# Performance work log

Hardware: AMD Instinct MI355X
Metric: run time of the kernel (lower is better)

## Reference

```python
import jax, jax.numpy as jnp
import numpy as np

N0, N1, N2 = 120000, 24000, 6000  # nodes per sampled layer
H1, C1 = 8, 64   # layer1: heads, nhid (concat -> 512)
H2, C2 = 8, 256  # layer2: out heads, code_embed_dim (mean over heads)
D = 256
NEG_SLOPE = 0.2


def gat_conv(x_src, x_dst, src, dst, W, att_src, att_dst, bias, n_tgt, concat):
    H, C = att_src.shape
    h_src = (x_src @ W).reshape(-1, H, C)   # [N_src, H, C]
    h_dst = (x_dst @ W).reshape(-1, H, C)   # [N_tgt, H, C]
    a_src = jnp.einsum('nhc,hc->nh', h_src, att_src)  # [N_src, H]
    a_dst = jnp.einsum('nhc,hc->nh', h_dst, att_dst)  # [N_tgt, H]
    e = a_src[src] + a_dst[dst]                       # [E, H]
    e = jnp.where(e > 0, e, NEG_SLOPE * e)            # LeakyReLU
    # segment softmax over edges grouped by target node
    m = jax.ops.segment_max(e, dst, num_segments=n_tgt)  # [N_tgt, H]
    ex = jnp.exp(e - m[dst])
    denom = jax.ops.segment_sum(ex, dst, num_segments=n_tgt)
    alpha = ex / denom[dst]                           # [E, H]
    msg = alpha[:, :, None] * h_src[src]              # [E, H, C]
    out = jax.ops.segment_sum(msg, dst, num_segments=n_tgt)  # [N_tgt, H, C]
    if concat:
        return out.reshape(n_tgt, H * C) + bias
    return out.mean(axis=1) + bias


def setup_inputs() -> dict:
    key = jax.random.key(0)
    ks = jax.random.split(key, 12)
    E1, E2 = 384000, 96000
    g1 = 1.0 / np.sqrt(D)
    g2 = 1.0 / np.sqrt(H1 * C1)
    return {
        'x': jax.random.normal(ks[0], (N0, D), jnp.float32),
        'src1': jax.random.randint(ks[1], (E1,), 0, N0),
        'dst1': jax.random.randint(ks[2], (E1,), 0, N1),
        'src2': jax.random.randint(ks[3], (E2,), 0, N1),
        'dst2': jax.random.randint(ks[4], (E2,), 0, N2),
        'W1': jax.random.normal(ks[5], (D, H1 * C1), jnp.float32) * g1,
        'att_src1': jax.random.normal(ks[6], (H1, C1), jnp.float32) * 0.1,
        'att_dst1': jax.random.normal(ks[7], (H1, C1), jnp.float32) * 0.1,
        'b1': jnp.zeros((H1 * C1,), jnp.float32),
        'W2': jax.random.normal(ks[8], (H1 * C1, H2 * C2), jnp.float32) * g2,
        'att_src2': jax.random.normal(ks[9], (H2, C2), jnp.float32) * 0.1,
        'att_dst2': jax.random.normal(ks[10], (H2, C2), jnp.float32) * 0.1,
        'b2': jnp.zeros((C2,), jnp.float32),
    }


def reference(x, src1, dst1, src2, dst2, W1, att_src1, att_dst1, b1,
              W2, att_src2, att_dst2, b2):
    # layer 1: bipartite conv (x, x[:N1]), concat heads, then ELU
    x1 = gat_conv(x, x[:N1], src1, dst1, W1, att_src1, att_dst1, b1, N1, True)
    x1 = jax.nn.elu(x1)
    # layer 2: (x1, x1[:N2]), mean over heads
    x2 = gat_conv(x1, x1[:N2], src2, dst2, W2, att_src2, att_dst2, b2, N2, False)
    return x2
```

## Files before the change

### kernel.cpp

```cpp
#include <hip/hip_runtime.h>
#include <hip/hip_bf16.h>
#include <cstdint>

typedef __attribute__((ext_vector_type(8))) short short8;
typedef __attribute__((ext_vector_type(4))) float floatx4;
typedef __hip_bfloat16 bf16;
typedef unsigned short u16;

static constexpr int cN0 = 120000, cN1 = 24000, cN2 = 6000;
static constexpr int cD = 256, cHC1 = 512;
static constexpr int CH1 = 4800;

__device__ __forceinline__ float dot4(float4 a, float4 b) {
  return a.x * b.x + a.y * b.y + a.z * b.z + a.w * b.w;
}

__global__ __launch_bounds__(256)
void gat_w1t(const float* __restrict__ W1, u16* __restrict__ dst) {
  int t = blockIdx.x * 256 + threadIdx.x;
  if (t >= 512 * 256) return;
  int n = t >> 8, k = t & 255;
  bf16 v = bf16(W1[(size_t)k * 512 + n]);
  dst[t] = *(u16*)&v;
}

__global__ __launch_bounds__(256)
void gat_make_w2te(const float* __restrict__ W2, u16* __restrict__ out) {
  __shared__ u16 tile[32][33];
  int kt = blockIdx.x * 32, ct = blockIdx.y * 32, h = blockIdx.z;
  int tx = threadIdx.x & 31, ty4 = (threadIdx.x >> 5) * 4;
#pragma unroll
  for (int i = 0; i < 4; i++) {
    int k = kt + ty4 + i, c = ct + tx;
    bf16 v = bf16(W2[(size_t)k * 2048 + h * 256 + c]);
    tile[ty4 + i][tx] = *(u16*)&v;
  }
  __syncthreads();
#pragma unroll
  for (int i = 0; i < 4; i++) {
    int c = ct + ty4 + i, k = kt + tx;
    out[(size_t)c * 4096 + h * 512 + k] = tile[tx][ty4 + i];
  }
}

__global__ __launch_bounds__(256)
void gat_make_watt(const float* __restrict__ W, const float* __restrict__ atts,
                   const float* __restrict__ attd, float* __restrict__ ws,
                   float* __restrict__ wd, int K, int Ch, int ldw) {
  int lane = threadIdx.x & 63;
  int task = blockIdx.x * 4 + (threadIdx.x >> 6);
  if (task >= 8 * K) return;
  int h = task / K, k = task - h * K;
  const float* Wr = W + (size_t)k * ldw + h * Ch;
  const float* as = atts + h * Ch;
  const float* ad = attd + h * Ch;
  float ss = 0.f, dd = 0.f;
  for (int c = lane; c < Ch; c += 64) {
    float wv = Wr[c];
    ss += wv * as[c];
    dd += wv * ad[c];
  }
#pragma unroll
  for (int o = 32; o; o >>= 1) { ss += __shfl_down(ss, o); dd += __shfl_down(dd, o); }
  if (lane == 0) { ws[task] = ss; wd[task] = dd; }
}

#define RSTAGE(HALF, MASK)                                              \
  {                                                                     \
    _Pragma("unroll") for (int j = 0; j < HALF; j++) {                  \
      float send = (lane & MASK) ? v[j] : v[j + HALF];                  \
      float rcv = __shfl_xor(send, MASK);                               \
      v[j] = ((lane & MASK) ? v[j + HALF] : v[j]) + rcv;                \
    }                                                                   \
  }

__global__ __launch_bounds__(256)
void gat_scores_reg(const float* __restrict__ x, const float* __restrict__ wsrc,
                    const float* __restrict__ wdst, float* __restrict__ a_s,
                    float* __restrict__ a_d, int M, int MD) {
  int lane = threadIdx.x & 63;
  int wv = (blockIdx.x * 256 + threadIdx.x) >> 6;
  int nw = (gridDim.x * 256) >> 6;
  float4 w[16];
#pragma unroll
  for (int j = 0; j < 8; j++) {
    w[j]     = *(const float4*)&wsrc[j * 256 + lane * 4];
    w[j + 8] = *(const float4*)&wdst[j * 256 + lane * 4];
  }
  for (int row = wv; row < M; row += nw) {
    float4 xv = *(const float4*)&x[(size_t)row * 256 + lane * 4];
    float v[16];
#pragma unroll
    for (int j = 0; j < 16; j++) v[j] = dot4(xv, w[j]);
    RSTAGE(8, 1) RSTAGE(4, 2) RSTAGE(2, 4) RSTAGE(1, 8)
    v[0] += __shfl_xor(v[0], 16);
    v[0] += __shfl_xor(v[0], 32);
    if (lane < 16) {
      int o = ((lane & 1) << 3) | ((lane & 2) << 1) | ((lane & 4) >> 1) | ((lane & 8) >> 3);
      if (o < 8) a_s[row * 8 + o] = v[0];
      else if (row < MD) a_d[row * 8 + (o - 8)] = v[0];
    }
  }
}

__global__ __launch_bounds__(256)
void gat_scores_w512(const float* __restrict__ x, const float* __restrict__ wsrc,
                     const float* __restrict__ wdst, float* __restrict__ a_s,
                     float* __restrict__ a_d, int M, int MD) {
  __shared__ float wl[16 * 512];
  int tid = threadIdx.x;
#pragma unroll
  for (int base = 0; base < 8192; base += 1024) {
    int idx = base + tid * 4;
    int j = idx >> 9, c = idx & 511;
    *(float4*)&wl[idx] = (j < 8) ? *(const float4*)&wsrc[j * 512 + c]
                                 : *(const float4*)&wdst[(j - 8) * 512 + c];
  }
  __syncthreads();
  int lane = tid & 63;
  int wv = (blockIdx.x * 256 + tid) >> 6;
  int nw = (gridDim.x * 256) >> 6;
  for (int row = wv; row < M; row += nw) {
    float4 xa = *(const float4*)&x[(size_t)row * 512 + lane * 4];
    float4 xb = *(const float4*)&x[(size_t)row * 512 + 256 + lane * 4];
    float v[16];
#pragma unroll
    for (int j = 0; j < 16; j++) {
      float4 wa = *(const float4*)&wl[j * 512 + lane * 4];
      float4 wb = *(const float4*)&wl[j * 512 + 256 + lane * 4];
      v[j] = dot4(xa, wa) + dot4(xb, wb);
    }
    RSTAGE(8, 1) RSTAGE(4, 2) RSTAGE(2, 4) RSTAGE(1, 8)
    v[0] += __shfl_xor(v[0], 16);
    v[0] += __shfl_xor(v[0], 32);
    if (lane < 16) {
      int o = ((lane & 1) << 3) | ((lane & 2) << 1) | ((lane & 4) >> 1) | ((lane & 8) >> 3);
      if (o < 8) a_s[row * 8 + o] = v[0];
      else if (row < MD) a_d[row * 8 + (o - 8)] = v[0];
    }
  }
}

__global__ __launch_bounds__(256)
void gat_hist(const int* __restrict__ dstv, int* __restrict__ cnt, int E) {
  int t = blockIdx.x * 256 + threadIdx.x;
  if (t < E) atomicAdd(&cnt[dstv[t]], 1);
}

__global__ __launch_bounds__(1024)
void gat_scan1(const int* __restrict__ cnt, int* __restrict__ off,
               int* __restrict__ bsum, int n) {
  __shared__ int wsum[16];
  int t = threadIdx.x, lane = t & 63, wid = t >> 6;
  int idx = blockIdx.x * 1024 + t;
  int v = (idx < n) ? cnt[idx] : 0;
  int x = v;
#pragma unroll
  for (int d = 1; d < 64; d <<= 1) { int y = __shfl_up(x, d); if (lane >= d) x += y; }
  if (lane == 63) wsum[wid] = x;
  __syncthreads();
  if (t < 16) {
    int s = wsum[t];
#pragma unroll
    for (int d = 1; d < 16; d <<= 1) { int y = __shfl_up(s, d); if (t >= d) s += y; }
    wsum[t] = s;
  }
  __syncthreads();
  int excl = (wid ? wsum[wid - 1] : 0) + x - v;
  if (idx < n) off[idx] = excl;
  if (t == 1023) bsum[blockIdx.x] = wsum[15];
}

__global__ __launch_bounds__(64)
void gat_scan2(int* __restrict__ bsum, int nb, int* __restrict__ off, int n) {
  int t = threadIdx.x;
  int v = (t < nb) ? bsum[t] : 0;
  int x = v;
#pragma unroll
  for (int d = 1; d < 64; d <<= 1) { int y = __shfl_up(x, d); if (t >= d) x += y; }
  if (t < nb) bsum[t] = x - v;
  if (t == 63) off[n] = x;
}

__global__ __launch_bounds__(256)
void gat_scan3(int* __restrict__ off, const int* __restrict__ bsum, int n) {
  int i = blockIdx.x * 256 + threadIdx.x;
  if (i < n) off[i] += bsum[i >> 10];
}

__global__ __launch_bounds__(256)
void gat_scatter_edge(const int* __restrict__ src, const int* __restrict__ dstv,
                      const float* __restrict__ a_s, const float* __restrict__ a_d,
                      const int* __restrict__ off, int* __restrict__ cur,
                      int* __restrict__ srcs, float* __restrict__ exs, int E) {
  int t = blockIdx.x * 256 + threadIdx.x;
  if (t >= E) return;
  int s = src[t], d = dstv[t];
  int slot = off[d] + atomicAdd(&cur[d], 1);
  srcs[slot] = s;
  const float* as = a_s + (size_t)s * 8;
  const float* ad = a_d + (size_t)d * 8;
  float4 s0 = *(const float4*)as, s1 = *(const float4*)(as + 4);
  float4 d0 = *(const float4*)ad, d1 = *(const float4*)(ad + 4);
  float ev[8] = { s0.x + d0.x, s0.y + d0.y, s0.z + d0.z, s0.w + d0.w,
                  s1.x + d1.x, s1.y + d1.y, s1.z + d1.z, s1.w + d1.w };
  float exv[8];
#pragma unroll
  for (int h = 0; h < 8; h++) {
    float e = ev[h];
    e = e > 0.f ? e : 0.2f * e;
    exv[h] = expf(e);
  }
  float4* op = (float4*)(exs + (size_t)slot * 8);
  op[0] = make_float4(exv[0], exv[1], exv[2], exv[3]);
  op[1] = make_float4(exv[4], exv[5], exv[6], exv[7]);
}

__global__ __launch_bounds__(256)
void gat_gather_in1(const float* __restrict__ x, const float* __restrict__ exs,
                    const int* __restrict__ off, const int* __restrict__ srcs,
                    u16* __restrict__ agg, int d0) {
  int d = d0 + blockIdx.x, t = threadIdx.x;
  int beg = off[d], end = off[d + 1];
  float acc[8] = {}, den[8] = {};
  int i = beg;
  if ((end - beg) & 1) {
    int s = srcs[i];
    float ea[8];
    *(float4*)&ea[0] = *(const float4*)&exs[(size_t)i * 8];
    *(float4*)&ea[4] = *(const float4*)&exs[(size_t)i * 8 + 4];
    float xv = x[(size_t)s * cD + t];
#pragma unroll
    for (int j = 0; j < 8; j++) { acc[j] += ea[j] * xv; den[j] += ea[j]; }
    i++;
  }
  for (; i < end; i += 2) {
    int s0 = srcs[i], s1 = srcs[i + 1];
    float ea[8], eb[8];
    *(float4*)&ea[0] = *(const float4*)&exs[(size_t)i * 8];
    *(float4*)&ea[4] = *(const float4*)&exs[(size_t)i * 8 + 4];
    *(float4*)&eb[0] = *(const float4*)&exs[(size_t)(i + 1) * 8];
    *(float4*)&eb[4] = *(const float4*)&exs[(size_t)(i + 1) * 8 + 4];
    float xv0 = x[(size_t)s0 * cD + t];
    float xv1 = x[(size_t)s1 * cD + t];
#pragma unroll
    for (int j = 0; j < 8; j++) {
      acc[j] += ea[j] * xv0 + eb[j] * xv1;
      den[j] += ea[j] + eb[j];
    }
  }
  u16* ap = agg + (size_t)blockIdx.x * 2048 + t;
#pragma unroll
  for (int j = 0; j < 8; j++) {
    float inv = den[j] > 0.f ? 1.f / den[j] : 0.f;
    bf16 v = bf16(acc[j] * inv);
    ap[(size_t)j * 256] = *(u16*)&v;
  }
}

__global__ __launch_bounds__(256)
void gat_gather_in2(const float* __restrict__ x1, const float* __restrict__ exs,
                    const int* __restrict__ off, const int* __restrict__ srcs,
                    u16* __restrict__ agg, int d0) {
  int d = d0 + blockIdx.x, t = threadIdx.x;
  int beg = off[d], end = off[d + 1];
  float acc0[8] = {}, acc1[8] = {}, den[8] = {};
  int i = beg;
  if ((end - beg) & 1) {
    int s = srcs[i];
    float ea[8];
    *(float4*)&ea[0] = *(const float4*)&exs[(size_t)i * 8];
    *(float4*)&ea[4] = *(const float4*)&exs[(size_t)i * 8 + 4];
    float xa = x1[(size_t)s * cHC1 + t];
    float xb = x1[(size_t)s * cHC1 + t + 256];
#pragma unroll
    for (int j = 0; j < 8; j++) { acc0[j] += ea[j] * xa; acc1[j] += ea[j] * xb; den[j] += ea[j]; }
    i++;
  }
  for (; i < end; i += 2) {
    int s0 = srcs[i], s1 = srcs[i + 1];
    float ea[8], eb[8];
    *(float4*)&ea[0] = *(const float4*)&exs[(size_t)i * 8];
    *(float4*)&ea[4] = *(const float4*)&exs[(size_t)i * 8 + 4];
    *(float4*)&eb[0] = *(const float4*)&exs[(size_t)(i + 1) * 8];
    *(float4*)&eb[4] = *(const float4*)&exs[(size_t)(i + 1) * 8 + 4];
    float xa0 = x1[(size_t)s0 * cHC1 + t];
    float xb0 = x1[(size_t)s0 * cHC1 + t + 256];
    float xa1 = x1[(size_t)s1 * cHC1 + t];
    float xb1 = x1[(size_t)s1 * cHC1 + t + 256];
#pragma unroll
    for (int j = 0; j < 8; j++) {
      acc0[j] += ea[j] * xa0 + eb[j] * xa1;
      acc1[j] += ea[j] * xb0 + eb[j] * xb1;
      den[j] += ea[j] + eb[j];
    }
  }
  u16* ap = agg + (size_t)blockIdx.x * 4096;
#pragma unroll
  for (int j = 0; j < 8; j++) {
    float inv = den[j] > 0.f ? 1.f / den[j] : 0.f;
    bf16 v0 = bf16(acc0[j] * inv), v1 = bf16(acc1[j] * inv);
    ap[(size_t)j * 512 + t]       = *(u16*)&v0;
    ap[(size_t)j * 512 + t + 256] = *(u16*)&v1;
  }
}

template<int BN, int EPI>
__global__ __launch_bounds__(256)
void gat_gemm(const u16* __restrict__ A, long lda, const u16* __restrict__ Bt, long ldb,
              float* __restrict__ C, long ldc, int M, int K,
              const float* __restrict__ bias, int zA, int zB, long zC, int zBias) {
  __shared__ __align__(16) u16 Al[64 * 64];
  __shared__ __align__(16) u16 Bl[BN * 64];
  const int tid = threadIdx.x;
  const int bm = blockIdx.x << 6;
  const int n0 = blockIdx.y * BN;
  const int z = blockIdx.z;
  const u16* Ab = A + (size_t)z * zA;
  const u16* Bb = Bt + (size_t)z * zB + (size_t)n0 * ldb;
  const int wid = tid >> 6, lane = tid & 63;
  const int wm = (wid & 1) << 5, wn = (wid >> 1) * (BN / 2);
  const int q = lane >> 4, r = lane & 15;
  constexpr int NJ = BN / 32;
  floatx4 acc[2][NJ] = {};
  const int arow = tid >> 3;
  const int chunk = tid & 7;
  const int acol = chunk << 3;
  for (int k0 = 0; k0 < K; k0 += 64) {
    __syncthreads();
#pragma unroll
    for (int rr = 0; rr < 2; rr++) {
      int row = arow + rr * 32;
      int gr = bm + row; if (gr >= M) gr = M - 1;
      *(uint4*)&Al[row * 64 + ((chunk ^ (row & 7)) << 3)] =
          *(const uint4*)&Ab[(size_t)gr * lda + k0 + acol];
    }
#pragma unroll
    for (int rr = 0; rr < BN / 32; rr++) {
      int row = arow + rr * 32;
      *(uint4*)&Bl[row * 64 + ((chunk ^ (row & 7)) << 3)] =
          *(const uint4*)&Bb[(size_t)row * ldb + k0 + acol];
    }
    __syncthreads();
#pragma unroll
    for (int kk = 0; kk < 64; kk += 32) {
      const int cs = (((kk >> 3) + q) ^ (r & 7)) << 3;
      short8 af[2], bfr[NJ];
#pragma unroll
      for (int i = 0; i < 2; i++)  af[i]  = *(const short8*)&Al[(wm + i * 16 + r) * 64 + cs];
#pragma unroll
      for (int j = 0; j < NJ; j++) bfr[j] = *(const short8*)&Bl[(wn + j * 16 + r) * 64 + cs];
#pragma unroll
      for (int i = 0; i < 2; i++)
#pragma unroll
        for (int j = 0; j < NJ; j++)
          acc[i][j] = __builtin_amdgcn_mfma_f32_16x16x32_bf16(af[i], bfr[j], acc[i][j], 0, 0, 0);
    }
  }
#pragma unroll
  for (int i = 0; i < 2; i++)
#pragma unroll
    for (int j = 0; j < NJ; j++) {
      int gn = n0 + wn + j * 16 + r;
      float bv = (EPI == 1) ? bias[zBias * z + gn] : 0.f;
#pragma unroll
      for (int t2 = 0; t2 < 4; t2++) {
        int gm = bm + wm + i * 16 + q * 4 + t2;
        if (gm < M) {
          float v = acc[i][j][t2];
          if (EPI == 1) { v += bv; v = v > 0.f ? v : expm1f(v); }
          C[(size_t)z * zC + (size_t)gm * ldc + gn] = v;
        }
      }
    }
}

__global__ __launch_bounds__(256)
void gat_reduce4(const float* __restrict__ p, const float* __restrict__ bias,
                 float* __restrict__ out, int MN) {
  int t = blockIdx.x * 256 + threadIdx.x;
  if (t >= MN) return;
  size_t mn = (size_t)MN;
  float v = p[t] + p[t + mn] + p[t + 2 * mn] + p[t + 3 * mn];
  out[t] = v * 0.125f + bias[t & 255];
}

extern "C" void kernel_launch(void* const* d_in, const int* in_sizes, int n_in,
                              void* d_out, int out_size, void* d_ws, size_t ws_size,
                              hipStream_t stream) {
  const float* x    = (const float*)d_in[0];
  const int* src1   = (const int*)d_in[1];
  const int* dst1   = (const int*)d_in[2];
  const int* src2   = (const int*)d_in[3];
  const int* dst2   = (const int*)d_in[4];
  const float* W1   = (const float*)d_in[5];
  const float* atts1 = (const float*)d_in[6];
  const float* attd1 = (const float*)d_in[7];
  const float* b1   = (const float*)d_in[8];
  const float* W2   = (const float*)d_in[9];
  const float* atts2 = (const float*)d_in[10];
  const float* attd2 = (const float*)d_in[11];
  const float* b2   = (const float*)d_in[12];
  const int E1 = in_sizes[1], E2 = in_sizes[3];

  uint8_t* p = (uint8_t*)d_ws;
  auto alloc = [&](size_t b) { uint8_t* r = p; p += (b + 255) & ~(size_t)255; return r; };
  auto al = [](size_t b) { return (b + 255) & ~(size_t)255; };
  float* x1   = (float*)alloc((size_t)cN1 * cHC1 * 4);
  u16*   W1t  = (u16*)alloc((size_t)512 * 256 * 2);
  u16*   W2te = (u16*)alloc((size_t)256 * 4096 * 2);
  float* wts1 = (float*)alloc(8 * 256 * 4);
  float* wtd1 = (float*)alloc(8 * 256 * 4);
  float* wts2 = (float*)alloc(8 * 512 * 4);
  float* wtd2 = (float*)alloc(8 * 512 * 4);
  uint8_t* scratch = p;
  size_t usedPersist = (size_t)(scratch - (uint8_t*)d_ws);

  auto phaseA = [&](size_t m1) {
    return al(m1 * 2048 * 2) + al((size_t)cN0 * 32) + al((size_t)cN1 * 32) +
           al((size_t)E1 * 32) + al((size_t)E1 * 4) + al((size_t)(cN1 + 1) * 4) +
           al(256) + 2 * al((size_t)cN1 * 4);
  };
  int M1 = (usedPersist + phaseA(cN1) <= ws_size) ? cN1 : CH1;
  int nch1 = cN1 / M1;
  u16*   aggA  = (u16*)alloc((size_t)M1 * 2048 * 2);
  float* a_s1  = (float*)alloc((size_t)cN0 * 32);
  float* a_d1  = (float*)alloc((size_t)cN1 * 32);
  float* exs1  = (float*)alloc((size_t)E1 * 32);
  int*   srcs1 = (int*)alloc((size_t)E1 * 4);
  int*   off1  = (int*)alloc((size_t)(cN1 + 1) * 4);
  int*   bsum1 = (int*)alloc(256);
  uint8_t* zA = p;
  int*   cnt1 = (int*)alloc((size_t)cN1 * 4);
  int*   cur1 = (int*)alloc((size_t)cN1 * 4);
  size_t zAbytes = (size_t)(p - zA);

  auto phaseB = [&](size_t m2) {
    return al(m2 * 4096 * 2) + al(4ull * m2 * 256 * 4) + al((size_t)cN1 * 32) +
           al((size_t)cN2 * 32) + al((size_t)E2 * 32) + al((size_t)E2 * 4) +
           al((size_t)(cN2 + 1) * 4) + al(256) + 2 * al((size_t)cN2 * 4);
  };
  int M2 = (usedPersist + phaseB(6000) <= ws_size) ? 6000 : 3000;
  int nch2 = 6000 / M2;
  p = scratch;
  u16*   aggB  = (u16*)alloc((size_t)M2 * 4096 * 2);
  float* pbuf  = (float*)alloc(4ull * M2 * 256 * 4);
  float* a_s2  = (float*)alloc((size_t)cN1 * 32);
  float* a_d2  = (float*)alloc((size_t)cN2 * 32);
  float* exs2  = (float*)alloc((size_t)E2 * 32);
  int*   srcs2 = (int*)alloc((size_t)E2 * 4);
  int*   off2  = (int*)alloc((size_t)(cN2 + 1) * 4);
  int*   bsum2 = (int*)alloc(256);
  uint8_t* zB = p;
  int*   cnt2 = (int*)alloc((size_t)cN2 * 4);
  int*   cur2 = (int*)alloc((size_t)cN2 * 4);
  size_t zBbytes = (size_t)(p - zB);

  gat_w1t<<<(512 * 256 + 255) / 256, 256, 0, stream>>>(W1, W1t);
  gat_make_w2te<<<dim3(16, 8, 8), 256, 0, stream>>>(W2, W2te);
  gat_make_watt<<<2 * 256, 256, 0, stream>>>(W1, atts1, attd1, wts1, wtd1, 256, 64, 512);
  gat_make_watt<<<2 * 512, 256, 0, stream>>>(W2, atts2, attd2, wts2, wtd2, 512, 256, 2048);

  hipMemsetAsync(zA, 0, zAbytes, stream);
  gat_scores_reg<<<1024, 256, 0, stream>>>(x, wts1, wtd1, a_s1, a_d1, cN0, cN1);
  gat_hist<<<(E1 + 255) / 256, 256, 0, stream>>>(dst1, cnt1, E1);
  {
    int nb = (cN1 + 1023) / 1024;
    gat_scan1<<<nb, 1024, 0, stream>>>(cnt1, off1, bsum1, cN1);
    gat_scan2<<<1, 64, 0, stream>>>(bsum1, nb, off1, cN1);
    gat_scan3<<<(cN1 + 255) / 256, 256, 0, stream>>>(off1, bsum1, cN1);
  }
  gat_scatter_edge<<<(E1 + 255) / 256, 256, 0, stream>>>(src1, dst1, a_s1, a_d1, off1, cur1, srcs1, exs1, E1);
  for (int c = 0; c < nch1; c++) {
    int d0 = c * M1;
    gat_gather_in1<<<M1, 256, 0, stream>>>(x, exs1, off1, srcs1, aggA, d0);
    gat_gemm<64, 1><<<dim3(M1 / 64, 1, 8), 256, 0, stream>>>(
        aggA, 2048, W1t, 256, x1 + (size_t)d0 * cHC1, cHC1,
        M1, 256, b1, 256, 64 * 256, 64, 64);
  }

  hipMemsetAsync(zB, 0, zBbytes, stream);
  gat_scores_w512<<<512, 256, 0, stream>>>(x1, wts2, wtd2, a_s2, a_d2, cN1, cN2);
  gat_hist<<<(E2 + 255) / 256, 256, 0, stream>>>(dst2, cnt2, E2);
  {
    int nb = (cN2 + 1023) / 1024;
    gat_scan1<<<nb, 1024, 0, stream>>>(cnt2, off2, bsum2, cN2);
    gat_scan2<<<1, 64, 0, stream>>>(bsum2, nb, off2, cN2);
    gat_scan3<<<(cN2 + 255) / 256, 256, 0, stream>>>(off2, bsum2, cN2);
  }
  gat_scatter_edge<<<(E2 + 255) / 256, 256, 0, stream>>>(src2, dst2, a_s2, a_d2, off2, cur2, srcs2, exs2, E2);
  for (int c = 0; c < nch2; c++) {
    int d0 = c * M2;
    gat_gather_in2<<<M2, 256, 0, stream>>>(x1, exs2, off2, srcs2, aggB, d0);
    gat_gemm<128, 0><<<dim3((M2 + 63) / 64, 2, 4), 256, 0, stream>>>(
        aggB, 4096, W2te, 4096, pbuf, 256,
        M2, 1024, nullptr, 1024, 1024, (long)M2 * 256, 0);
    gat_reduce4<<<(M2 * 256 + 255) / 256, 256, 0, stream>>>(
        pbuf, b2, (float*)d_out + (size_t)d0 * 256, M2 * 256);
  }
}
```

Measured before the change: 495.4 us.

## Merge prep kernels, fold scan stages, split softmax denominator from gather

Combines the four weight-preparation kernels into one launch and merges the second and third scan stages so each block sums the per-block partials itself. It also moves the softmax denominator into a separate per-node kernel and rewrites the gather as one templated kernel that unrolls four edges per iteration. Layer 2 now uses 512 threads per node instead of two columns per thread. The intent is to cut launch count and raise memory-level parallelism in the gathers, at the cost of an extra denominator pass and extra den buffers.

Measured after the change: 483.9 us. 2.3% less time.

```diff
diff --git a/kernel.cpp b/kernel.cpp
--- a/kernel.cpp
+++ b/kernel.cpp
@@ -16,49 +16,63 @@
 }
 
 __global__ __launch_bounds__(256)
-void gat_w1t(const float* __restrict__ W1, u16* __restrict__ dst) {
-  int t = blockIdx.x * 256 + threadIdx.x;
-  if (t >= 512 * 256) return;
-  int n = t >> 8, k = t & 255;
-  bf16 v = bf16(W1[(size_t)k * 512 + n]);
-  dst[t] = *(u16*)&v;
-}
-
-__global__ __launch_bounds__(256)
-void gat_make_w2te(const float* __restrict__ W2, u16* __restrict__ out) {
+void gat_prep(const float* __restrict__ W1, const float* __restrict__ W2,
+              const float* __restrict__ as1, const float* __restrict__ ad1,
+              const float* __restrict__ as2, const float* __restrict__ ad2,
+              u16* __restrict__ W1t, u16* __restrict__ W2te,
+              float* __restrict__ wts1, float* __restrict__ wtd1,
+              float* __restrict__ wts2, float* __restrict__ wtd2) {
   __shared__ u16 tile[32][33];
-  int kt = blockIdx.x * 32, ct = blockIdx.y * 32, h = blockIdx.z;
-  int tx = threadIdx.x & 31, ty4 = (threadIdx.x >> 5) * 4;
-#pragma unroll
-  for (int i = 0; i < 4; i++) {
-    int k = kt + ty4 + i, c = ct + tx;
-    bf16 v = bf16(W2[(size_t)k * 2048 + h * 256 + c]);
-    tile[ty4 + i][tx] = *(u16*)&v;
-  }
-  __syncthreads();
-#pragma unroll
-  for (int i = 0; i < 4; i++) {
-    int c = ct + ty4 + i, k = kt + tx;
-    out[(size_t)c * 4096 + h * 512 + k] = tile[tx][ty4 + i];
-  }
-}
-
-__global__ __launch_bounds__(256)
-void gat_make_watt(const float* __restrict__ W, const float* __restrict__ atts,
-                   const float* __restrict__ attd, float* __restrict__ ws,
-                   float* __restrict__ wd, int K, int Ch, int ldw) {
+  int b = (int)blockIdx.x;
+  if (b < 512) {
+    int t = b * 256 + threadIdx.x;
+    int n = t >> 8, k = t & 255;
+    bf16 v = bf16(W1[(size_t)k * 512 + n]);
+    W1t[t] = *(u16*)&v;
+    return;
+  }
+  b -= 512;
+  if (b < 1024) {
+    int bx = b & 15, by = (b >> 4) & 7, h = b >> 7;
+    int kt = bx * 32, ct = by * 32;
+    int tx = threadIdx.x & 31, ty4 = (threadIdx.x >> 5) * 4;
+#pragma unroll
+    for (int i = 0; i < 4; i++) {
+      int k = kt + ty4 + i, c = ct + tx;
+      bf16 v = bf16(W2[(size_t)k * 2048 + h * 256 + c]);
+      tile[ty4 + i][tx] = *(u16*)&v;
+    }
+    __syncthreads();
+#pragma unroll
+    for (int i = 0; i < 4; i++) {
+      int c = ct + ty4 + i, k = kt + tx;
+      W2te[(size_t)c * 4096 + h * 512 + k] = tile[tx][ty4 + i];
+    }
+    return;
+  }
+  b -= 1024;
   int lane = threadIdx.x & 63;
-  int task = blockIdx.x * 4 + (threadIdx.x >> 6);
+  int K, Ch, ldw, task;
+  const float *W, *as, *ad;
+  float *ws, *wd;
+  if (b < 512) {
+    K = 256; Ch = 64; ldw = 512; W = W1; as = as1; ad = ad1; ws = wts1; wd = wtd1;
+    task = b * 4 + (threadIdx.x >> 6);
+  } else {
+    b -= 512;
+    K = 512; Ch = 256; ldw = 2048; W = W2; as = as2; ad = ad2; ws = wts2; wd = wtd2;
+    task = b * 4 + (threadIdx.x >> 6);
+  }
   if (task >= 8 * K) return;
   int h = task / K, k = task - h * K;
   const float* Wr = W + (size_t)k * ldw + h * Ch;
-  const float* as = atts + h * Ch;
-  const float* ad = attd + h * Ch;
+  const float* asp = as + h * Ch;
+  const float* adp = ad + h * Ch;
   float ss = 0.f, dd = 0.f;
   for (int c = lane; c < Ch; c += 64) {
     float wv = Wr[c];
-    ss += wv * as[c];
-    dd += wv * ad[c];
+    ss += wv * asp[c];
+    dd += wv * adp[c];
   }
 #pragma unroll
   for (int o = 32; o; o >>= 1) { ss += __shfl_down(ss, o); dd += __shfl_down(dd, o); }
@@ -171,21 +185,18 @@
   if (t == 1023) bsum[blockIdx.x] = wsum[15];
 }
 
-__global__ __launch_bounds__(64)
-void gat_scan2(int* __restrict__ bsum, int nb, int* __restrict__ off, int n) {
-  int t = threadIdx.x;
-  int v = (t < nb) ? bsum[t] : 0;
-  int x = v;
-#pragma unroll
-  for (int d = 1; d < 64; d <<= 1) { int y = __shfl_up(x, d); if (t >= d) x += y; }
-  if (t < nb) bsum[t] = x - v;
-  if (t == 63) off[n] = x;
-}
-
-__global__ __launch_bounds__(256)
-void gat_scan3(int* __restrict__ off, const int* __restrict__ bsum, int n) {
+__global__ __launch_bounds__(256)
+void gat_scan3(int* __restrict__ off, const int* __restrict__ bsum, int n, int nb) {
   int i = blockIdx.x * 256 + threadIdx.x;
-  if (i < n) off[i] += bsum[i >> 10];
+  int blk = (blockIdx.x * 256) >> 10;
+  int add = 0;
+  for (int b = 0; b < blk; b++) add += bsum[b];
+  if (i < n) off[i] += add;
+  if (i == 0) {
+    int tot = 0;
+    for (int b = 0; b < nb; b++) tot += bsum[b];
+    off[n] = tot;
+  }
 }
 
 __global__ __launch_bounds__(256)
@@ -217,91 +228,72 @@
 }
 
 __global__ __launch_bounds__(256)
-void gat_gather_in1(const float* __restrict__ x, const float* __restrict__ exs,
-                    const int* __restrict__ off, const int* __restrict__ srcs,
-                    u16* __restrict__ agg, int d0) {
+void gat_denom(const float* __restrict__ exs, const int* __restrict__ off,
+               float* __restrict__ den, int N) {
+  int lane = threadIdx.x & 63;
+  int d = blockIdx.x * 4 + (threadIdx.x >> 6);
+  if (d >= N) return;
+  int beg = off[d], end = off[d + 1];
+  float s = 0.f;
+  for (size_t idx = (size_t)beg * 8 + lane; idx < (size_t)end * 8; idx += 64)
+    s += exs[idx];
+#pragma unroll
+  for (int o = 32; o >= 8; o >>= 1) s += __shfl_down(s, o);
+  if (lane < 8) den[(size_t)d * 8 + lane] = s;
+}
+
+template<int CDIM>
+__global__ __launch_bounds__(CDIM)
+void gat_gather(const float* __restrict__ x, const float* __restrict__ exs,
+                const float* __restrict__ den, const int* __restrict__ off,
+                const int* __restrict__ srcs, u16* __restrict__ agg, int d0) {
   int d = d0 + blockIdx.x, t = threadIdx.x;
   int beg = off[d], end = off[d + 1];
-  float acc[8] = {}, den[8] = {};
+  float inv[8];
+#pragma unroll
+  for (int j = 0; j < 8; j++) {
+    float dv = den[(size_t)d * 8 + j];
+    inv[j] = dv > 0.f ? 1.f / dv : 0.f;
+  }
+  float acc[8] = {};
+  const float* xb = x + t;
   int i = beg;
-  if ((end - beg) & 1) {
+  for (; i + 4 <= end; i += 4) {
+    int s0 = srcs[i], s1 = srcs[i + 1], s2 = srcs[i + 2], s3 = srcs[i + 3];
+    float xv0 = xb[(size_t)s0 * CDIM];
+    float xv1 = xb[(size_t)s1 * CDIM];
+    float xv2 = xb[(size_t)s2 * CDIM];
+    float xv3 = xb[(size_t)s3 * CDIM];
+    float4 e0a = *(const float4*)&exs[(size_t)i * 8];
+    float4 e0b = *(const float4*)&exs[(size_t)i * 8 + 4];
+    float4 e1a = *(const float4*)&exs[(size_t)(i + 1) * 8];
+    float4 e1b = *(const float4*)&exs[(size_t)(i + 1) * 8 + 4];
+    float4 e2a = *(const float4*)&exs[(size_t)(i + 2) * 8];
+    float4 e2b = *(const float4*)&exs[(size_t)(i + 2) * 8 + 4];
+    float4 e3a = *(const float4*)&exs[(size_t)(i + 3) * 8];
+    float4 e3b = *(const float4*)&exs[(size_t)(i + 3) * 8 + 4];
+    acc[0] += e0a.x * xv0 + e1a.x * xv1 + e2a.x * xv2 + e3a.x * xv3;
+    acc[1] += e0a.y * xv0 + e1a.y * xv1 + e2a.y * xv2 + e3a.y * xv3;
+    acc[2] += e0a.z * xv0 + e1a.z * xv1 + e2a.z * xv2 + e3a.z * xv3;
+    acc[3] += e0a.w * xv0 + e1a.w * xv1 + e2a.w * xv2 + e3a.w * xv3;
+    acc[4] += e0b.x * xv0 + e1b.x * xv1 + e2b.x * xv2 + e3b.x * xv3;
+    acc[5] += e0b.y * xv0 + e1b.y * xv1 + e2b.y * xv2 + e3b.y * xv3;
+    acc[6] += e0b.z * xv0 + e1b.z * xv1 + e2b.z * xv2 + e3b.z * xv3;
+    acc[7] += e0b.w * xv0 + e1b.w * xv1 + e2b.w * xv2 + e3b.w * xv3;
+  }
+  for (; i < end; i++) {
     int s = srcs[i];
-    float ea[8];
-    *(float4*)&ea[0] = *(const float4*)&exs[(size_t)i * 8];
-    *(float4*)&ea[4] = *(const float4*)&exs[(size_t)i * 8 + 4];
-    float xv = x[(size_t)s * cD + t];
-#pragma unroll
-    for (int j = 0; j < 8; j++) { acc[j] += ea[j] * xv; den[j] += ea[j]; }
-    i++;
-  }
-  for (; i < end; i += 2) {
-    int s0 = srcs[i], s1 = srcs[i + 1];
-    float ea[8], eb[8];
-    *(float4*)&ea[0] = *(const float4*)&exs[(size_t)i * 8];
-    *(float4*)&ea[4] = *(const float4*)&exs[(size_t)i * 8 + 4];
-    *(float4*)&eb[0] = *(const float4*)&exs[(size_t)(i + 1) * 8];
-    *(float4*)&eb[4] = *(const float4*)&exs[(size_t)(i + 1) * 8 + 4];
-    float xv0 = x[(size_t)s0 * cD + t];
-    float xv1 = x[(size_t)s1 * cD + t];
-#pragma unroll
-    for (int j = 0; j < 8; j++) {
-      acc[j] += ea[j] * xv0 + eb[j] * xv1;
-      den[j] += ea[j] + eb[j];
-    }
-  }
-  u16* ap = agg + (size_t)blockIdx.x * 2048 + t;
+    float xv = xb[(size_t)s * CDIM];
+    float4 ea = *(const float4*)&exs[(size_t)i * 8];
+    float4 eb = *(const float4*)&exs[(size_t)i * 8 + 4];
+    acc[0] += ea.x * xv; acc[1] += ea.y * xv; acc[2] += ea.z * xv; acc[3] += ea.w * xv;
+    acc[4] += eb.x * xv; acc[5] += eb.y * xv; acc[6] += eb.z * xv; acc[7] += eb.w * xv;
+  }
+  u16* ap = agg + (size_t)blockIdx.x * (8 * CDIM) + t;
 #pragma unroll
   for (int j = 0; j < 8; j++) {
-    float inv = den[j] > 0.f ? 1.f / den[j] : 0.f;
-    bf16 v = bf16(acc[j] * inv);
-    ap[(size_t)j * 256] = *(u16*)&v;
-  }
-}
-
-__global__ __launch_bounds__(256)
-void gat_gather_in2(const float* __restrict__ x1, const float* __restrict__ exs,
-                    const int* __restrict__ off, const int* __restrict__ srcs,
-                    u16* __restrict__ agg, int d0) {
-  int d = d0 + blockIdx.x, t = threadIdx.x;
-  int beg = off[d], end = off[d + 1];
-  float acc0[8] = {}, acc1[8] = {}, den[8] = {};
-  int i = beg;
-  if ((end - beg) & 1) {
-    int s = srcs[i];
-    float ea[8];
-    *(float4*)&ea[0] = *(const float4*)&exs[(size_t)i * 8];
-    *(float4*)&ea[4] = *(const float4*)&exs[(size_t)i * 8 + 4];
-    float xa = x1[(size_t)s * cHC1 + t];
-    float xb = x1[(size_t)s * cHC1 + t + 256];
-#pragma unroll
-    for (int j = 0; j < 8; j++) { acc0[j] += ea[j] * xa; acc1[j] += ea[j] * xb; den[j] += ea[j]; }
-    i++;
-  }
-  for (; i < end; i += 2) {
-    int s0 = srcs[i], s1 = srcs[i + 1];
-    float ea[8], eb[8];
-    *(float4*)&ea[0] = *(const float4*)&exs[(size_t)i * 8];
-    *(float4*)&ea[4] = *(const float4*)&exs[(size_t)i * 8 + 4];
-    *(float4*)&eb[0] = *(const float4*)&exs[(size_t)(i + 1) * 8];
-    *(float4*)&eb[4] = *(const float4*)&exs[(size_t)(i + 1) * 8 + 4];
-    float xa0 = x1[(size_t)s0 * cHC1 + t];
-    float xb0 = x1[(size_t)s0 * cHC1 + t + 256];
-    float xa1 = x1[(size_t)s1 * cHC1 + t];
-    float xb1 = x1[(size_t)s1 * cHC1 + t + 256];
-#pragma unroll
-    for (int j = 0; j < 8; j++) {
-      acc0[j] += ea[j] * xa0 + eb[j] * xa1;
-      acc1[j] += ea[j] * xb0 + eb[j] * xb1;
-      den[j] += ea[j] + eb[j];
-    }
-  }
-  u16* ap = agg + (size_t)blockIdx.x * 4096;
-#pragma unroll
-  for (int j = 0; j < 8; j++) {
-    float inv = den[j] > 0.f ? 1.f / den[j] : 0.f;
-    bf16 v0 = bf16(acc0[j] * inv), v1 = bf16(acc1[j] * inv);
-    ap[(size_t)j * 512 + t]       = *(u16*)&v0;
-    ap[(size_t)j * 512 + t + 256] = *(u16*)&v1;
+    bf16 v = bf16(acc[j] * inv[j]);
+    ap[(size_t)j * CDIM] = *(u16*)&v;
   }
 }
 
@@ -419,7 +411,7 @@
   auto phaseA = [&](size_t m1) {
     return al(m1 * 2048 * 2) + al((size_t)cN0 * 32) + al((size_t)cN1 * 32) +
            al((size_t)E1 * 32) + al((size_t)E1 * 4) + al((size_t)(cN1 + 1) * 4) +
-           al(256) + 2 * al((size_t)cN1 * 4);
+           al(256) + al((size_t)cN1 * 32) + 2 * al((size_t)cN1 * 4);
   };
   int M1 = (usedPersist + phaseA(cN1) <= ws_size) ? cN1 : CH1;
   int nch1 = cN1 / M1;
@@ -430,6 +422,7 @@
   int*   srcs1 = (int*)alloc((size_t)E1 * 4);
   int*   off1  = (int*)alloc((size_t)(cN1 + 1) * 4);
   int*   bsum1 = (int*)alloc(256);
+  float* den1  = (float*)alloc((size_t)cN1 * 32);
   uint8_t* zA = p;
   int*   cnt1 = (int*)alloc((size_t)cN1 * 4);
   int*   cur1 = (int*)alloc((size_t)cN1 * 4);
@@ -438,7 +431,8 @@
   auto phaseB = [&](size_t m2) {
     return al(m2 * 4096 * 2) + al(4ull * m2 * 256 * 4) + al((size_t)cN1 * 32) +
            al((size_t)cN2 * 32) + al((size_t)E2 * 32) + al((size_t)E2 * 4) +
-           al((size_t)(cN2 + 1) * 4) + al(256) + 2 * al((size_t)cN2 * 4);
+           al((size_t)(cN2 + 1) * 4) + al(256) + al((size_t)cN2 * 32) +
+           2 * al((size_t)cN2 * 4);
   };
   int M2 = (usedPersist + phaseB(6000) <= ws_size) ? 6000 : 3000;
   int nch2 = 6000 / M2;
@@ -451,15 +445,14 @@
   int*   srcs2 = (int*)alloc((size_t)E2 * 4);
   int*   off2  = (int*)alloc((size_t)(cN2 + 1) * 4);
   int*   bsum2 = (int*)alloc(256);
+  float* den2  = (float*)alloc((size_t)cN2 * 32);
   uint8_t* zB = p;
   int*   cnt2 = (int*)alloc((size_t)cN2 * 4);
   int*   cur2 = (int*)alloc((size_t)cN2 * 4);
   size_t zBbytes = (size_t)(p - zB);
 
-  gat_w1t<<<(512 * 256 + 255) / 256, 256, 0, stream>>>(W1, W1t);
-  gat_make_w2te<<<dim3(16, 8, 8), 256, 0, stream>>>(W2, W2te);
-  gat_make_watt<<<2 * 256, 256, 0, stream>>>(W1, atts1, attd1, wts1, wtd1, 256, 64, 512);
-  gat_make_watt<<<2 * 512, 256, 0, stream>>>(W2, atts2, attd2, wts2, wtd2, 512, 256, 2048);
+  gat_prep<<<3072, 256, 0, stream>>>(W1, W2, atts1, attd1, atts2, attd2,
+                                     W1t, W2te, wts1, wtd1, wts2, wtd2);
 
   hipMemsetAsync(zA, 0, zAbytes, stream);
   gat_scores_reg<<<1024, 256, 0, stream>>>(x, wts1, wtd1, a_s1, a_d1, cN0, cN1);
@@ -467,13 +460,13 @@
   {
     int nb = (cN1 + 1023) / 1024;
     gat_scan1<<<nb, 1024, 0, stream>>>(cnt1, off1, bsum1, cN1);
-    gat_scan2<<<1, 64, 0, stream>>>(bsum1, nb, off1, cN1);
-    gat_scan3<<<(cN1 + 255) / 256, 256, 0, stream>>>(off1, bsum1, cN1);
+    gat_scan3<<<(cN1 + 255) / 256, 256, 0, stream>>>(off1, bsum1, cN1, nb);
   }
   gat_scatter_edge<<<(E1 + 255) / 256, 256, 0, stream>>>(src1, dst1, a_s1, a_d1, off1, cur1, srcs1, exs1, E1);
+  gat_denom<<<(cN1 + 3) / 4, 256, 0, stream>>>(exs1, off1, den1, cN1);
   for (int c = 0; c < nch1; c++) {
     int d0 = c * M1;
-    gat_gather_in1<<<M1, 256, 0, stream>>>(x, exs1, off1, srcs1, aggA, d0);
+    gat_gather<256><<<M1, 256, 0, stream>>>(x, exs1, den1, off1, srcs1, aggA, d0);
     gat_gemm<64, 1><<<dim3(M1 / 64, 1, 8), 256, 0, stream>>>(
         aggA, 2048, W1t, 256, x1 + (size_t)d0 * cHC1, cHC1,
         M1, 256, b1, 256, 64 * 256, 64, 64);
@@ -485,13 +478,13 @@
   {
     int nb = (cN2 + 1023) / 1024;
     gat_scan1<<<nb, 1024, 0, stream>>>(cnt2, off2, bsum2, cN2);
-    gat_scan2<<<1, 64, 0, stream>>>(bsum2, nb, off2, cN2);
-    gat_scan3<<<(cN2 + 255) / 256, 256, 0, stream>>>(off2, bsum2, cN2);
+    gat_scan3<<<(cN2 + 255) / 256, 256, 0, stream>>>(off2, bsum2, cN2, nb);
   }
   gat_scatter_edge<<<(E2 + 255) / 256, 256, 0, stream>>>(src2, dst2, a_s2, a_d2, off2, cur2, srcs2, exs2, E2);
+  gat_denom<<<(cN2 + 3) / 4, 256, 0, stream>>>(exs2, off2, den2, cN2);
   for (int c = 0; c < nch2; c++) {
     int d0 = c * M2;
-    gat_gather_in2<<<M2, 256, 0, stream>>>(x1, exs2, off2, srcs2, aggB, d0);
+    gat_gather<512><<<M2, 512, 0, stream>>>(x1, exs2, den2, off2, srcs2, aggB, d0);
     gat_gemm<128, 0><<<dim3((M2 + 63) / 64, 2, 4), 256, 0, stream>>>(
         aggB, 4096, W2te, 4096, pbuf, 256,
         M2, 1024, nullptr, 1024, 1024, (long)M2 * 256, 0);
```
